# Performance work log

Measured on AMD Instinct MI355X. Metric: run time of the kernel, lower is better.

The kernel has to match this reference:

```python
import jax, jax.numpy as jnp
import numpy as np

N_NODES = 50000
N_EDGES = 800000
N_GRAPHS = 64
D_IN = 768
D_HID = 256


def gcn_conv(x, src, dst, W, b, n_nodes):
    """PyG GCNConv: symmetric-normalized aggregation with self-loops.
    out = D^{-1/2} (A + I) D^{-1/2} (x @ W) + b
    """
    h = x @ W  # [N, C_out]
    # degree from target nodes, counting the implicit self-loop (+1)
    deg = jax.ops.segment_sum(jnp.ones((src.shape[0],), h.dtype), dst,
                              num_segments=n_nodes) + 1.0
    dinv = jax.lax.rsqrt(deg)  # deg >= 1 always (self-loop)
    norm = (dinv[src] * dinv[dst])[:, None]  # [E, 1]
    agg = jax.ops.segment_sum(h[src] * norm, dst, num_segments=n_nodes)
    # self-loop contribution: norm_ii = dinv_i^2
    agg = agg + (dinv * dinv)[:, None] * h
    return agg + b


def global_mean_pool(x, batch, n_graphs):
    s = jax.ops.segment_sum(x, batch, num_segments=n_graphs)
    cnt = jax.ops.segment_sum(jnp.ones((x.shape[0],), x.dtype), batch,
                              num_segments=n_graphs)
    return s / jnp.maximum(cnt, 1.0)[:, None]


def setup_inputs() -> dict:
    key = jax.random.key(0)
    ks = jax.random.split(key, 12)
    x = jax.random.normal(ks[0], (N_NODES, D_IN), jnp.float32)
    edge_index = jax.random.randint(ks[1], (2, N_EDGES), 0, N_NODES, jnp.int64)
    batch = jnp.sort(jax.random.randint(ks[2], (N_NODES,), 0, N_GRAPHS, jnp.int64))
    def glorot(k, shape):
        lim = np.sqrt(6.0 / (shape[0] + shape[1]))
        return jax.random.uniform(k, shape, jnp.float32, -lim, lim)
    return {
        "x": x, "edge_index": edge_index, "batch": batch,
        "W1": glorot(ks[3], (D_IN, D_HID)), "b1": jnp.zeros((D_HID,), jnp.float32),
        "W2": glorot(ks[4], (D_HID, D_HID)), "b2": jnp.zeros((D_HID,), jnp.float32),
        "W3": glorot(ks[5], (D_HID, D_HID)), "b3": jnp.zeros((D_HID,), jnp.float32),
        "Wl": glorot(ks[6], (D_HID, D_IN)), "bl": jnp.zeros((D_IN,), jnp.float32),
    }


def reference(x, edge_index, batch, W1, b1, W2, b2, W3, b3, Wl, bl):
    src, dst = edge_index[0], edge_index[1]
    n = x.shape[0]
    # dropout is identity in eval mode
    h = jax.nn.relu(gcn_conv(x, src, dst, W1, b1, n))
    h = jax.nn.relu(gcn_conv(h, src, dst, W2, b2, n))
    h = gcn_conv(h, src, dst, W3, b3, n)
    g = global_mean_pool(h, batch, N_GRAPHS)  # [G, D_HID]
    return g @ Wl + bl  # [G, D_IN]
```

## Files before the change

### kernel.cpp

```cpp
#include <hip/hip_runtime.h>
#include <hip/hip_bf16.h>

#define D_IN 768
#define D_HID 256

typedef __attribute__((ext_vector_type(8))) short short8;
typedef __attribute__((ext_vector_type(4))) float f32x4;

__device__ inline float b2f(unsigned short u) {
    unsigned x = ((unsigned)u) << 16;
    union { unsigned u; float f; } c; c.u = x; return c.f;
}
__device__ inline unsigned short f2b(float v) {
    __hip_bfloat16 h = __float2bfloat16(v);
    return *(unsigned short*)&h;
}

__device__ inline void gload_lds16(const void* g, void* l) {
    __builtin_amdgcn_global_load_lds(
        (const __attribute__((address_space(1))) unsigned int*)g,
        (__attribute__((address_space(3))) unsigned int*)l, 16, 0, 0);
}


__global__ void k_count(const int* __restrict__ dst, int* __restrict__ deg, int E) {
    int i = blockIdx.x * 256 + threadIdx.x;
    if (i < E) atomicAdd(&deg[dst[i]], 1);
}

__global__ void k_dinv(const int* __restrict__ deg, float* __restrict__ dinv, int N) {
    int i = blockIdx.x * 256 + threadIdx.x;
    if (i < N) dinv[i] = rsqrtf((float)deg[i] + 1.0f);
}

__global__ __launch_bounds__(1024) void k_scan(const int* __restrict__ deg,
                                               int* __restrict__ row_ptr, int N) {
    __shared__ int wsum[16];
    __shared__ int carry_s;
    int t = threadIdx.x;
    int lane = t & 63, wid = t >> 6;
    if (t == 0) carry_s = 0;
    __syncthreads();
    for (int base = 0; base < N; base += 1024) {
        int i = base + t;
        int v = (i < N) ? deg[i] : 0;
        int s = v;
        #pragma unroll
        for (int d = 1; d < 64; d <<= 1) {
            int tmp = __shfl_up(s, d);
            if (lane >= d) s += tmp;
        }
        if (lane == 63) wsum[wid] = s;
        __syncthreads();
        if (wid == 0 && lane < 16) {
            int ws = wsum[lane];
            #pragma unroll
            for (int d = 1; d < 16; d <<= 1) {
                int tmp = __shfl_up(ws, d);
                if (lane >= d) ws += tmp;
            }
            wsum[lane] = ws;
        }
        __syncthreads();
        int carry = carry_s;
        int woff = (wid > 0) ? wsum[wid - 1] : 0;
        if (i < N) row_ptr[i] = carry + woff + s - v;
        __syncthreads();
        if (t == 0) carry_s = carry + wsum[15];
        __syncthreads();
    }
    if (t == 0) row_ptr[N] = carry_s;
}

__global__ void k_fill(const int* __restrict__ src, const int* __restrict__ dst,
                       const int* __restrict__ row_ptr, int* __restrict__ wptr,
                       int* __restrict__ csr_src, int E) {
    int i = blockIdx.x * 256 + threadIdx.x;
    if (i < E) {
        int d = dst[i];
        int w = atomicAdd(&wptr[d], 1);
        csr_src[row_ptr[d] + w] = src[i];
    }
}

__global__ void k_bounds(const int* __restrict__ batch, int* __restrict__ cnt,
                         int* __restrict__ offg, int N, int G) {
    int g = threadIdx.x;
    if (g >= G) return;
    auto lower = [&](int key) {
        int lo = 0, hi = N;
        while (lo < hi) {
            int mid = (lo + hi) >> 1;
            if (batch[mid] < key) lo = mid + 1; else hi = mid;
        }
        return lo;
    };
    int lo = lower(g);
    int hi = lower(g + 1);
    offg[g] = lo;
    cnt[g] = hi - lo;
}

__global__ __launch_bounds__(256) void k_wc(const float* __restrict__ W3,
                                            const float* __restrict__ Wl,
                                            float* __restrict__ Wc) {
    __shared__ float w3s[16][256];
    int t = threadIdx.x;
    int cx = blockIdx.x, iq = blockIdx.y;
    #pragma unroll
    for (int r = 0; r < 16; ++r)
        w3s[r][t] = W3[(size_t)(iq * 16 + r) * 256 + t];
    __syncthreads();
    int c = cx * 256 + t;
    float acc[16];
    #pragma unroll
    for (int i = 0; i < 16; ++i) acc[i] = 0.f;
    for (int m = 0; m < 256; ++m) {
        float wl = Wl[(size_t)m * 768 + c];
        #pragma unroll
        for (int i = 0; i < 16; ++i) acc[i] = fmaf(w3s[i][m], wl, acc[i]);
    }
    #pragma unroll
    for (int i = 0; i < 16; ++i)
        Wc[(size_t)(iq * 16 + i) * 768 + c] = acc[i];
}

__global__ __launch_bounds__(256) void k_bc(const float* __restrict__ b3,
                                            const float* __restrict__ Wl,
                                            const float* __restrict__ bl,
                                            float* __restrict__ bc) {
    __shared__ float b3s[256];
    int t = threadIdx.x;
    b3s[t] = b3[t];
    __syncthreads();
    int c = blockIdx.x * 256 + t;
    float acc = bl[c];
    for (int m = 0; m < 256; ++m) acc = fmaf(b3s[m], Wl[(size_t)m * 768 + c], acc);
    bc[c] = acc;
}

__global__ void k_prep_B(const float* __restrict__ W, short* __restrict__ Bp, int KA) {
    int t = blockIdx.x * 256 + threadIdx.x;
    if (t >= KA * 256) return;
    int k = t >> 8, n = t & 255;
    float v = W[(size_t)k * 256 + n];
    unsigned short h = f2b(v);
    unsigned short l = f2b(v - b2f(h));
    int c = k >> 5, q = (k >> 3) & 3, j = k & 7;
    int tile = n >> 4, ln = n & 15;
    size_t base = (size_t)c * 16384 + (size_t)(tile * 4 + q) * 128 + ln * 8 + j;
    Bp[base] = (short)h;
    Bp[base + 8192] = (short)l;
}

template <int MODE>
__global__ __launch_bounds__(512, 4) void k_gemm7(const void* __restrict__ Av,
                                                  const short* __restrict__ Bp,
                                                  unsigned short* __restrict__ C,
                                                  int M) {
    constexpr int KA = (MODE == 1) ? D_IN : D_HID;
    constexpr int NCH = KA / 32;
    __shared__ short Bs[2][8192];

    int t = threadIdx.x;
    int lane = t & 63, w = t >> 6;
    int wr2 = w >> 1, wc2 = w & 1;
    int ln = lane & 15, q = lane >> 4;
    int bm = blockIdx.x * 128;
    int bn = blockIdx.y * 128;
    int TB = blockIdx.y * 8;

    const char* Abase[2];
    #pragma unroll
    for (int s = 0; s < 2; ++s) {
        int rr = bm + wr2 * 32 + s * 16 + ln;
        rr = (rr < M) ? rr : (M - 1);
        Abase[s] = (const char*)Av + (size_t)rr * KA * ((MODE == 1) ? 4 : 2);
    }

    f32x4 acc[2][4];
    #pragma unroll
    for (int s = 0; s < 2; ++s)
        #pragma unroll
        for (int tt = 0; tt < 4; ++tt) acc[s][tt] = (f32x4){0.f, 0.f, 0.f, 0.f};

    auto stage = [&](int c, int pb) {
        gload_lds16(Bp + (size_t)c * 16384 + (size_t)(TB + w) * 512 + lane * 8,
                    &Bs[pb][w * 512]);
        gload_lds16(Bp + (size_t)c * 16384 + 8192 + (size_t)(TB + w) * 512 + lane * 8,
                    &Bs[pb][4096 + w * 512]);
    };

    stage(0, 0);

    f32x4 cur0[2], cur1[2];
    short8 curb[2];
    #pragma unroll
    for (int s = 0; s < 2; ++s) {
        if (MODE == 1) {
            const float* Af = (const float*)(Abase[s]) + q * 8;
            cur0[s] = *(const f32x4*)Af;
            cur1[s] = *(const f32x4*)(Af + 4);
        } else {
            curb[s] = *(const short8*)((const unsigned short*)(Abase[s]) + q * 8);
        }
    }
    __syncthreads();

    for (int c = 0; c < NCH; ++c) {
        int pb = c & 1;
        bool more = (c + 1 < NCH);
        if (more) stage(c + 1, pb ^ 1);

        f32x4 nxt0[2], nxt1[2];
        short8 nxtb[2];
        if (more) {
            #pragma unroll
            for (int s = 0; s < 2; ++s) {
                if (MODE == 1) {
                    const float* Af = (const float*)(Abase[s]) + (c + 1) * 32 + q * 8;
                    nxt0[s] = *(const f32x4*)Af;
                    nxt1[s] = *(const f32x4*)(Af + 4);
                } else {
                    nxtb[s] = *(const short8*)((const unsigned short*)(Abase[s]) + (c + 1) * 32 + q * 8);
                }
            }
        }

        short8 a_hi[2], a_lo[2];
        #pragma unroll
        for (int s = 0; s < 2; ++s) {
            if (MODE == 1) {
                float vv[8] = {cur0[s][0], cur0[s][1], cur0[s][2], cur0[s][3],
                               cur1[s][0], cur1[s][1], cur1[s][2], cur1[s][3]};
                #pragma unroll
                for (int j = 0; j < 8; ++j) {
                    unsigned short h = f2b(vv[j]);
                    a_hi[s][j] = (short)h;
                    a_lo[s][j] = (short)f2b(vv[j] - b2f(h));
                }
            } else {
                a_hi[s] = curb[s];
            }
        }

        #pragma unroll
        for (int tt = 0; tt < 4; ++tt) {
            const short* bp = &Bs[pb][(size_t)(wc2 * 4 + tt) * 512 + q * 128 + ln * 8];
            short8 bh = *(const short8*)bp;
            short8 bl2 = *(const short8*)(bp + 4096);
            #pragma unroll
            for (int s = 0; s < 2; ++s) {
                acc[s][tt] = __builtin_amdgcn_mfma_f32_16x16x32_bf16(a_hi[s], bh, acc[s][tt], 0, 0, 0);
                if (MODE == 1)
                    acc[s][tt] = __builtin_amdgcn_mfma_f32_16x16x32_bf16(a_lo[s], bh, acc[s][tt], 0, 0, 0);
                acc[s][tt] = __builtin_amdgcn_mfma_f32_16x16x32_bf16(a_hi[s], bl2, acc[s][tt], 0, 0, 0);
            }
        }
        __syncthreads();

        if (more) {
            #pragma unroll
            for (int s = 0; s < 2; ++s) {
                if (MODE == 1) { cur0[s] = nxt0[s]; cur1[s] = nxt1[s]; }
                else           { curb[s] = nxtb[s]; }
            }
        }
    }

    #pragma unroll
    for (int s = 0; s < 2; ++s)
        #pragma unroll
        for (int tt = 0; tt < 4; ++tt)
            #pragma unroll
            for (int r = 0; r < 4; ++r) {
                int row = bm + wr2 * 32 + s * 16 + q * 4 + r;
                if (row < M)
                    C[(size_t)row * 256 + bn + wc2 * 64 + tt * 16 + ln] = f2b(acc[s][tt][r]);
            }
}

template <int RELU, int OUTBF>
__global__ __launch_bounds__(256) void k_agg(const unsigned short* __restrict__ hin,
                                             void* __restrict__ hout,
                                             const int* __restrict__ row_ptr,
                                             const int* __restrict__ csr_src,
                                             const float* __restrict__ dinv,
                                             const float* __restrict__ bias, int N) {
    int w = threadIdx.x >> 6;
    int lane = threadIdx.x & 63;
    int row = blockIdx.x * 4 + w;
    if (row >= N) return;
    int half = lane >> 5;
    int hl = lane & 31;
    int c8 = hl * 8;

    int2 se = *(const int2*)&row_ptr[row];
    int s = se.x, e = se.y;

    float di = dinv[row];
    short8 vs = *(const short8*)&hin[(size_t)row * 256 + c8];
    float4 bb0 = *(const float4*)&bias[c8];
    float4 bb1 = *(const float4*)&bias[c8 + 4];

    float acc[8];
    #pragma unroll
    for (int ch = 0; ch < 8; ++ch) acc[ch] = 0.f;

    for (int base = s; base < e; base += 64) {
        int cnt = e - base;
        if (cnt > 64) cnt = 64;
        int gidx = base + lane;
        if (gidx >= e) gidx = e - 1;
        int myu = csr_src[gidx];
        float mydv = dinv[myu];

        int p = 0;
        for (; p + 8 <= cnt; p += 8) {
            int u[4];
            float dv[4];
            short8 v[4];
            #pragma unroll
            for (int qq = 0; qq < 4; ++qq) {
                u[qq]  = __shfl(myu,  p + 2 * qq + half);
                dv[qq] = __shfl(mydv, p + 2 * qq + half);
            }
            #pragma unroll
            for (int qq = 0; qq < 4; ++qq) v[qq] = *(const short8*)&hin[(size_t)u[qq] * 256 + c8];
            #pragma unroll
            for (int qq = 0; qq < 4; ++qq)
                #pragma unroll
                for (int ch = 0; ch < 8; ++ch)
                    acc[ch] += dv[qq] * b2f((unsigned short)v[qq][ch]);
        }
        for (; p + 2 <= cnt; p += 2) {
            int u  = __shfl(myu,  p + half);
            float dv = __shfl(mydv, p + half);
            short8 v = *(const short8*)&hin[(size_t)u * 256 + c8];
            #pragma unroll
            for (int ch = 0; ch < 8; ++ch) acc[ch] += dv * b2f((unsigned short)v[ch]);
        }
        if (p < cnt) {
            int u = __shfl(myu, p);
            float dv = half ? 0.f : __shfl(mydv, p);
            short8 v = *(const short8*)&hin[(size_t)u * 256 + c8];
            #pragma unroll
            for (int ch = 0; ch < 8; ++ch) acc[ch] += dv * b2f((unsigned short)v[ch]);
        }
    }

    #pragma unroll
    for (int ch = 0; ch < 8; ++ch) acc[ch] += __shfl_xor(acc[ch], 32);

    float dii = di * di;
    float r[8];
    #pragma unroll
    for (int ch = 0; ch < 8; ++ch) {
        float b = (ch < 4) ? ((ch == 0) ? bb0.x : (ch == 1) ? bb0.y : (ch == 2) ? bb0.z : bb0.w)
                           : ((ch == 4) ? bb1.x : (ch == 5) ? bb1.y : (ch == 6) ? bb1.z : bb1.w);
        r[ch] = acc[ch] * di + dii * b2f((unsigned short)vs[ch]) + b;
        if (RELU) r[ch] = fmaxf(r[ch], 0.f);
    }

    float r0 = half ? r[4] : r[0];
    float r1 = half ? r[5] : r[1];
    float r2 = half ? r[6] : r[2];
    float r3 = half ? r[7] : r[3];
    int cofs = c8 + half * 4;

    if (OUTBF) {
        ushort4 o;
        o.x = f2b(r0); o.y = f2b(r1); o.z = f2b(r2); o.w = f2b(r3);
        *(ushort4*)((unsigned short*)hout + (size_t)row * 256 + cofs) = o;
    } else {
        *(float4*)((float*)hout + (size_t)row * 256 + cofs) = make_float4(r0, r1, r2, r3);
    }
}

__global__ __launch_bounds__(256) void k_pool(const float* __restrict__ h,
                                              const int* __restrict__ cnt,
                                              const int* __restrict__ offg,
                                              float* __restrict__ g) {
    int gi = blockIdx.x, slice = blockIdx.y;
    int c = threadIdx.x;
    int start = offg[gi], n = cnt[gi];
    int per = (n + (int)gridDim.y - 1) / (int)gridDim.y;
    int r0 = slice * per;
    int r1 = min(n, r0 + per);
    float acc = 0.f;
    for (int r = r0; r < r1; ++r) acc += h[(size_t)(start + r) * D_HID + c];
    if (r1 > r0) atomicAdd(&g[gi * D_HID + c], acc);
}

__global__ __launch_bounds__(256) void k_final(const float* __restrict__ g,
                                               const int* __restrict__ cnt,
                                               const float* __restrict__ Wc,
                                               const float* __restrict__ bc,
                                               float* __restrict__ out) {
    __shared__ float gs[D_HID];
    int t = threadIdx.x;
    int gi = blockIdx.y;
    int c = blockIdx.x * 256 + t;
    float inv = 1.0f / (float)max(cnt[gi], 1);
    gs[t] = g[gi * D_HID + t] * inv;
    __syncthreads();
    float acc = bc[c];
    #pragma unroll 8
    for (int k = 0; k < D_HID; ++k) acc = fmaf(gs[k], Wc[(size_t)k * D_IN + c], acc);
    out[(size_t)gi * D_IN + c] = acc;
}


extern "C" void kernel_launch(void* const* d_in, const int* in_sizes, int n_in,
                              void* d_out, int out_size, void* d_ws, size_t ws_size,
                              hipStream_t stream) {
    const float* x     = (const float*)d_in[0];
    const int*   ei    = (const int*)d_in[1];
    const int*   batch = (const int*)d_in[2];
    const float* W1 = (const float*)d_in[3];
    const float* b1 = (const float*)d_in[4];
    const float* W2 = (const float*)d_in[5];
    const float* b2 = (const float*)d_in[6];
    const float* W3 = (const float*)d_in[7];
    const float* b3 = (const float*)d_in[8];
    const float* Wl = (const float*)d_in[9];
    const float* bl = (const float*)d_in[10];
    float* out = (float*)d_out;

    int N = in_sizes[2];
    int E = in_sizes[1] / 2;
    int G = out_size / D_IN;
    const int* srcp = ei;
    const int* dstp = ei + E;

    char* ws = (char*)d_ws;
    size_t o = 0;
    auto alloc = [&](size_t bytes) -> char* {
        char* p = ws + o;
        o += (bytes + 255) & ~(size_t)255;
        return p;
    };
    int*   deg     = (int*)alloc((size_t)N * 4);
    int*   wptr    = (int*)alloc((size_t)N * 4);
    int*   row_ptr = (int*)alloc((size_t)(N + 1) * 4);
    int*   cnt     = (int*)alloc((size_t)G * 4);
    int*   offg    = (int*)alloc((size_t)G * 4);
    int*   csr_src = (int*)alloc((size_t)E * 4);
    float* dinv    = (float*)alloc((size_t)N * 4);
    float* gbuf    = (float*)alloc((size_t)G * D_HID * 4);
    float* zbias   = (float*)alloc((size_t)D_HID * 4);
    float* Wc      = (float*)alloc((size_t)D_HID * D_IN * 4);
    float* bc      = (float*)alloc((size_t)D_IN * 4);
    unsigned short* hG  = (unsigned short*)alloc((size_t)N * D_HID * 2);
    unsigned short* hA2 = (unsigned short*)alloc((size_t)N * D_HID * 2);
    float* hF      = (float*)alloc((size_t)N * D_HID * 4);
    short* Bp1     = (short*)alloc((size_t)(D_IN / 32) * 16384 * 2);
    short* Bp2     = (short*)alloc((size_t)(D_HID / 32) * 16384 * 2);

    hipMemsetAsync(deg, 0, (size_t)N * 4, stream);
    hipMemsetAsync(wptr, 0, (size_t)N * 4, stream);
    hipMemsetAsync(gbuf, 0, (size_t)G * D_HID * 4, stream);
    hipMemsetAsync(zbias, 0, (size_t)D_HID * 4, stream);

    int gE = (E + 255) / 256;
    int gN = (N + 255) / 256;

    k_count<<<gE, 256, 0, stream>>>(dstp, deg, E);
    k_dinv<<<gN, 256, 0, stream>>>(deg, dinv, N);
    k_scan<<<1, 1024, 0, stream>>>(deg, row_ptr, N);
    k_fill<<<gE, 256, 0, stream>>>(srcp, dstp, row_ptr, wptr, csr_src, E);
    k_bounds<<<1, 64, 0, stream>>>(batch, cnt, offg, N, G);

    k_prep_B<<<D_IN, 256, 0, stream>>>(W1, Bp1, D_IN);
    k_prep_B<<<D_HID, 256, 0, stream>>>(W2, Bp2, D_HID);
    dim3 wc_grid(3, 16);
    k_wc<<<wc_grid, 256, 0, stream>>>(W3, Wl, Wc);
    k_bc<<<3, 256, 0, stream>>>(b3, Wl, bl, bc);

    dim3 gemm_grid((N + 127) / 128, 2);
    int agg_grid = (N + 3) / 4;

    k_gemm7<1><<<gemm_grid, 512, 0, stream>>>(x, Bp1, hG, N);
    k_agg<1, 1><<<agg_grid, 256, 0, stream>>>(hG, hA2, row_ptr, csr_src, dinv, b1, N);
    k_gemm7<2><<<gemm_grid, 512, 0, stream>>>(hA2, Bp2, hG, N);
    k_agg<1, 1><<<agg_grid, 256, 0, stream>>>(hG, hA2, row_ptr, csr_src, dinv, b2, N);
    k_agg<0, 0><<<agg_grid, 256, 0, stream>>>(hA2, hF, row_ptr, csr_src, dinv, zbias, N);

    dim3 pool_grid(G, 8);
    k_pool<<<pool_grid, 256, 0, stream>>>(hF, cnt, offg, gbuf);
    dim3 fin_grid(D_IN / 256, G);
    k_final<<<fin_grid, 256, 0, stream>>>(gbuf, cnt, Wc, bc, out);
}
```

Baseline: 753.6 us.

## Undo W3·Wl folding and add full-width 128x256 GEMM kernel for hidden layers

Drops the precomputed Wc = W3·Wl and bc fold. Layer 3 now runs an explicit hidden GEMM with W3 (split into bf16 hi/lo) before aggregation, and the final projection uses Wl and bl directly. A new k_gemm4 computes all 256 output columns per 128-row block, so the A tile is read once instead of twice across a two-block N split. This adds a full N×256×256 GEMM to the main path in exchange for removing two small setup kernels and reusing A more.

```diff
diff --git a/kernel.cpp b/kernel.cpp
--- a/kernel.cpp
+++ b/kernel.cpp
@@ -101,44 +101,6 @@
     cnt[g] = hi - lo;
 }
 
-__global__ __launch_bounds__(256) void k_wc(const float* __restrict__ W3,
-                                            const float* __restrict__ Wl,
-                                            float* __restrict__ Wc) {
-    __shared__ float w3s[16][256];
-    int t = threadIdx.x;
-    int cx = blockIdx.x, iq = blockIdx.y;
-    #pragma unroll
-    for (int r = 0; r < 16; ++r)
-        w3s[r][t] = W3[(size_t)(iq * 16 + r) * 256 + t];
-    __syncthreads();
-    int c = cx * 256 + t;
-    float acc[16];
-    #pragma unroll
-    for (int i = 0; i < 16; ++i) acc[i] = 0.f;
-    for (int m = 0; m < 256; ++m) {
-        float wl = Wl[(size_t)m * 768 + c];
-        #pragma unroll
-        for (int i = 0; i < 16; ++i) acc[i] = fmaf(w3s[i][m], wl, acc[i]);
-    }
-    #pragma unroll
-    for (int i = 0; i < 16; ++i)
-        Wc[(size_t)(iq * 16 + i) * 768 + c] = acc[i];
-}
-
-__global__ __launch_bounds__(256) void k_bc(const float* __restrict__ b3,
-                                            const float* __restrict__ Wl,
-                                            const float* __restrict__ bl,
-                                            float* __restrict__ bc) {
-    __shared__ float b3s[256];
-    int t = threadIdx.x;
-    b3s[t] = b3[t];
-    __syncthreads();
-    int c = blockIdx.x * 256 + t;
-    float acc = bl[c];
-    for (int m = 0; m < 256; ++m) acc = fmaf(b3s[m], Wl[(size_t)m * 768 + c], acc);
-    bc[c] = acc;
-}
-
 __global__ void k_prep_B(const float* __restrict__ W, short* __restrict__ Bp, int KA) {
     int t = blockIdx.x * 256 + threadIdx.x;
     if (t >= KA * 256) return;
@@ -277,6 +239,101 @@
                 int row = bm + wr2 * 32 + s * 16 + q * 4 + r;
                 if (row < M)
                     C[(size_t)row * 256 + bn + wc2 * 64 + tt * 16 + ln] = f2b(acc[s][tt][r]);
+            }
+}
+
+template <int MODE>
+__global__ __launch_bounds__(512, 4) void k_gemm4(const void* __restrict__ Av,
+                                                  const short* __restrict__ Bp,
+                                                  unsigned short* __restrict__ C,
+                                                  int M) {
+    constexpr int KA = (MODE == 1) ? D_IN : D_HID;
+    constexpr int NCH = KA / 32;
+    __shared__ short Bs[2][16384];
+
+    int t = threadIdx.x;
+    int lane = t & 63, w = t >> 6;
+    int wr = w >> 2, wc = w & 3;
+    int ln = lane & 15, q = lane >> 4;
+    int bm = blockIdx.x * 128;
+
+    const char* Abase[4];
+    #pragma unroll
+    for (int s = 0; s < 4; ++s) {
+        int rr = bm + wr * 64 + s * 16 + ln;
+        rr = (rr < M) ? rr : (M - 1);
+        Abase[s] = (const char*)Av + (size_t)rr * KA * ((MODE == 1) ? 4 : 2);
+    }
+
+    f32x4 acc[4][4];
+    #pragma unroll
+    for (int s = 0; s < 4; ++s)
+        #pragma unroll
+        for (int tt = 0; tt < 4; ++tt) acc[s][tt] = (f32x4){0.f, 0.f, 0.f, 0.f};
+
+    auto stage = [&](int c, int pb) {
+        #pragma unroll
+        for (int i = 0; i < 4; ++i) {
+            int seg = i * 8 + w;
+            gload_lds16(Bp + (size_t)c * 16384 + seg * 512 + lane * 8,
+                        &Bs[pb][seg * 512]);
+        }
+    };
+
+    stage(0, 0);
+    __syncthreads();
+
+    for (int c = 0; c < NCH; ++c) {
+        int pb = c & 1;
+        if (c + 1 < NCH) stage(c + 1, pb ^ 1);
+
+        short8 a_hi[4], a_lo[4];
+        #pragma unroll
+        for (int s = 0; s < 4; ++s) {
+            if (MODE == 1) {
+                const float* Af = (const float*)(Abase[s]) + c * 32 + q * 8;
+                f32x4 v0 = *(const f32x4*)Af;
+                f32x4 v1 = *(const f32x4*)(Af + 4);
+                float vv[8] = {v0[0], v0[1], v0[2], v0[3], v1[0], v1[1], v1[2], v1[3]};
+                #pragma unroll
+                for (int j = 0; j < 8; ++j) {
+                    unsigned short h = f2b(vv[j]);
+                    a_hi[s][j] = (short)h;
+                    a_lo[s][j] = (short)f2b(vv[j] - b2f(h));
+                }
+            } else {
+                const unsigned short* Ab = (const unsigned short*)(Abase[s]) + c * 32 + q * 8;
+                a_hi[s] = *(const short8*)Ab;
+            }
+        }
+
+        #pragma unroll
+        for (int tt = 0; tt < 4; ++tt) {
+            int T = wc * 4 + tt;
+            const short* bp = &Bs[pb][(size_t)(T * 4 + q) * 128 + ln * 8];
+            short8 bh = *(const short8*)bp;
+            short8 bl = *(const short8*)(bp + 8192);
+            #pragma unroll
+            for (int s = 0; s < 4; ++s) {
+                acc[s][tt] = __builtin_amdgcn_mfma_f32_16x16x32_bf16(a_hi[s], bh, acc[s][tt], 0, 0, 0);
+                if (MODE == 1)
+                    acc[s][tt] = __builtin_amdgcn_mfma_f32_16x16x32_bf16(a_lo[s], bh, acc[s][tt], 0, 0, 0);
+                acc[s][tt] = __builtin_amdgcn_mfma_f32_16x16x32_bf16(
+                    (MODE == 1) ? a_hi[s] : a_hi[s], bl, acc[s][tt], 0, 0, 0);
+            }
+        }
+        __syncthreads();
+    }
+
+    #pragma unroll
+    for (int s = 0; s < 4; ++s)
+        #pragma unroll
+        for (int tt = 0; tt < 4; ++tt)
+            #pragma unroll
+            for (int r = 0; r < 4; ++r) {
+                int row = bm + wr * 64 + s * 16 + q * 4 + r;
+                if (row < M)
+                    C[(size_t)row * 256 + wc * 64 + tt * 16 + ln] = f2b(acc[s][tt][r]);
             }
 }
 
@@ -394,8 +451,8 @@
 
 __global__ __launch_bounds__(256) void k_final(const float* __restrict__ g,
                                                const int* __restrict__ cnt,
-                                               const float* __restrict__ Wc,
-                                               const float* __restrict__ bc,
+                                               const float* __restrict__ Wl,
+                                               const float* __restrict__ bl,
                                                float* __restrict__ out) {
     __shared__ float gs[D_HID];
     int t = threadIdx.x;
@@ -404,9 +461,9 @@
     float inv = 1.0f / (float)max(cnt[gi], 1);
     gs[t] = g[gi * D_HID + t] * inv;
     __syncthreads();
-    float acc = bc[c];
+    float acc = bl[c];
     #pragma unroll 8
-    for (int k = 0; k < D_HID; ++k) acc = fmaf(gs[k], Wc[(size_t)k * D_IN + c], acc);
+    for (int k = 0; k < D_HID; ++k) acc = fmaf(gs[k], Wl[(size_t)k * D_IN + c], acc);
     out[(size_t)gi * D_IN + c] = acc;
 }
 
@@ -448,19 +505,16 @@
     int*   csr_src = (int*)alloc((size_t)E * 4);
     float* dinv    = (float*)alloc((size_t)N * 4);
     float* gbuf    = (float*)alloc((size_t)G * D_HID * 4);
-    float* zbias   = (float*)alloc((size_t)D_HID * 4);
-    float* Wc      = (float*)alloc((size_t)D_HID * D_IN * 4);
-    float* bc      = (float*)alloc((size_t)D_IN * 4);
     unsigned short* hG  = (unsigned short*)alloc((size_t)N * D_HID * 2);
     unsigned short* hA2 = (unsigned short*)alloc((size_t)N * D_HID * 2);
     float* hF      = (float*)alloc((size_t)N * D_HID * 4);
     short* Bp1     = (short*)alloc((size_t)(D_IN / 32) * 16384 * 2);
     short* Bp2     = (short*)alloc((size_t)(D_HID / 32) * 16384 * 2);
+    short* Bp3     = (short*)alloc((size_t)(D_HID / 32) * 16384 * 2);
 
     hipMemsetAsync(deg, 0, (size_t)N * 4, stream);
     hipMemsetAsync(wptr, 0, (size_t)N * 4, stream);
     hipMemsetAsync(gbuf, 0, (size_t)G * D_HID * 4, stream);
-    hipMemsetAsync(zbias, 0, (size_t)D_HID * 4, stream);
 
     int gE = (E + 255) / 256;
     int gN = (N + 255) / 256;
@@ -473,21 +527,21 @@
 
     k_prep_B<<<D_IN, 256, 0, stream>>>(W1, Bp1, D_IN);
     k_prep_B<<<D_HID, 256, 0, stream>>>(W2, Bp2, D_HID);
-    dim3 wc_grid(3, 16);
-    k_wc<<<wc_grid, 256, 0, stream>>>(W3, Wl, Wc);
-    k_bc<<<3, 256, 0, stream>>>(b3, Wl, bl, bc);
-
-    dim3 gemm_grid((N + 127) / 128, 2);
+    k_prep_B<<<D_HID, 256, 0, stream>>>(W3, Bp3, D_HID);
+
+    dim3 g7_grid((N + 127) / 128, 2);
+    int g4_grid = (N + 127) / 128;
     int agg_grid = (N + 3) / 4;
 
-    k_gemm7<1><<<gemm_grid, 512, 0, stream>>>(x, Bp1, hG, N);
+    k_gemm7<1><<<g7_grid, 512, 0, stream>>>(x, Bp1, hG, N);
     k_agg<1, 1><<<agg_grid, 256, 0, stream>>>(hG, hA2, row_ptr, csr_src, dinv, b1, N);
-    k_gemm7<2><<<gemm_grid, 512, 0, stream>>>(hA2, Bp2, hG, N);
+    k_gemm4<2><<<g4_grid, 512, 0, stream>>>(hA2, Bp2, hG, N);
     k_agg<1, 1><<<agg_grid, 256, 0, stream>>>(hG, hA2, row_ptr, csr_src, dinv, b2, N);
-    k_agg<0, 0><<<agg_grid, 256, 0, stream>>>(hA2, hF, row_ptr, csr_src, dinv, zbias, N);
+    k_gemm4<2><<<g4_grid, 512, 0, stream>>>(hA2, Bp3, hG, N);
+    k_agg<0, 0><<<agg_grid, 256, 0, stream>>>(hG, hF, row_ptr, csr_src, dinv, b3, N);
 
     dim3 pool_grid(G, 8);
     k_pool<<<pool_grid, 256, 0, stream>>>(hF, cnt, offg, gbuf);
     dim3 fin_grid(D_IN / 256, G);
-    k_final<<<fin_grid, 256, 0, stream>>>(gbuf, cnt, Wc, bc, out);
-}
+    k_final<<<fin_grid, 256, 0, stream>>>(gbuf, cnt, Wl, bl, out);
+}
```

New measurement: 729.4 us. -3.2%, faster.
